# Kernel tuning notes

Hardware: AMD Instinct MI355X
Metric: run time of the kernel (lower is better)

Reference implementation:

```python
import jax, jax.numpy as jnp
import numpy as np

B, L, D = 2, 2048, 2048
NH, NKV = 16, 8
HD = D // NH            # 128
GQ = NH // NKV          # queries per kv head
THETA = 10000.0
SCALE = HD ** -0.5


def rope_tables(seq_len, dim, theta):
    inv_freq = 1.0 / theta ** (jnp.arange(0, dim, 2, dtype=jnp.float32) / dim)
    t = jnp.arange(seq_len, dtype=jnp.float32)
    freqs = jnp.outer(t, inv_freq)              # [L, dim/2]
    emb = jnp.concatenate([freqs, freqs], -1)   # [L, dim]
    return jnp.cos(emb), jnp.sin(emb)


def rotate_half(x):
    x1, x2 = jnp.split(x, 2, axis=-1)
    return jnp.concatenate([-x2, x1], -1)


def setup_inputs() -> dict:
    key = jax.random.key(0)
    ks = jax.random.split(key, 5)
    s = 0.02
    return {
        "x": jax.random.normal(ks[0], (B, L, D), jnp.float32),
        "Wq": jax.random.normal(ks[1], (NH * HD, D), jnp.float32) * s,
        "Wk": jax.random.normal(ks[2], (NKV * HD, D), jnp.float32) * s,
        "Wv": jax.random.normal(ks[3], (NKV * HD, D), jnp.float32) * s,
        "Wo": jax.random.normal(ks[4], (D, D), jnp.float32) * s,
    }


def reference(x, Wq, Wk, Wv, Wo):
    b, l, d = x.shape
    q = (x @ Wq.T).reshape(b, l, NH, HD).transpose(0, 2, 1, 3)    # [B,NH,L,HD]
    k = (x @ Wk.T).reshape(b, l, NKV, HD).transpose(0, 2, 1, 3)   # [B,NKV,L,HD]
    v = (x @ Wv.T).reshape(b, l, NKV, HD).transpose(0, 2, 1, 3)

    cos, sin = rope_tables(l, HD, THETA)                           # [L,HD]
    q = q * cos + rotate_half(q) * sin
    k = k * cos + rotate_half(k) * sin

    # GQA without materializing expanded K/V: group queries per kv head
    qg = q.reshape(b, NKV, GQ, l, HD)
    scores = jnp.einsum('bgrld,bgmd->bgrlm', qg, k) * SCALE        # [B,NKV,GQ,L,L]
    causal = jnp.triu(jnp.ones((l, l), bool), k=1)
    scores = jnp.where(causal, -jnp.inf, scores)
    attn = jax.nn.softmax(scores.astype(jnp.float32), axis=-1).astype(q.dtype)
    out = jnp.einsum('bgrlm,bgmd->bgrld', attn, v)                 # [B,NKV,GQ,L,HD]
    out = out.reshape(b, NH, l, HD).transpose(0, 2, 1, 3).reshape(b, l, d)
    return out @ Wo.T
```

## Files before the change

kernel.cpp:

```cpp
#include <hip/hip_runtime.h>
#include <cmath>

using u16 = unsigned short;
typedef u16    u16x4  __attribute__((ext_vector_type(4)));
typedef u16    u16x8  __attribute__((ext_vector_type(8)));
typedef __bf16 bf16x8 __attribute__((ext_vector_type(8)));
typedef float  f32x4  __attribute__((ext_vector_type(4)));

constexpr int Bc  = 2;
constexpr int Lc  = 2048;
constexpr int Dc  = 2048;
constexpr int NHc = 16;
constexpr int NKVc= 8;
constexpr int HDc = 128;

__device__ __forceinline__ u16 f2b(float f) {
  union { float f; unsigned u; } v; v.f = f;
  unsigned r = v.u + 0x7FFFu + ((v.u >> 16) & 1u);
  return (u16)(r >> 16);
}
__device__ __forceinline__ u16 f2b_fast(float f) {
  union { float f; unsigned u; } v; v.f = f;
  return (u16)((v.u + 0x8000u) >> 16);
}
__device__ __forceinline__ float b2f(u16 s) {
  union { unsigned u; float f; } v; v.u = ((unsigned)s) << 16;
  return v.f;
}
__device__ __forceinline__ bf16x8 ld_frag(const u16* p) {
  u16x8 u = *(const u16x8*)p;
  return __builtin_bit_cast(bf16x8, u);
}
__device__ __forceinline__ void gld_lds16(u16* ldst, const u16* gsrc) {
  __builtin_amdgcn_global_load_lds(
      (const __attribute__((address_space(1))) void*)gsrc,
      (__attribute__((address_space(3))) void*)ldst, 16, 0, 0);
}

__global__ void cvt_f32_bf16(const float* __restrict__ src, u16* __restrict__ dst, int n) {
  int i = (blockIdx.x * blockDim.x + threadIdx.x) * 4;
  if (i >= n) return;
  float4 v = *(const float4*)&src[i];
  u16x4 o = { f2b(v.x), f2b(v.y), f2b(v.z), f2b(v.w) };
  *(u16x4*)&dst[i] = o;
}

__global__ void cvt_w3(const float* __restrict__ Wq, const float* __restrict__ Wk,
                       const float* __restrict__ Wv, u16* __restrict__ dst) {
  const int n1 = Dc * Dc;
  const int n2 = n1 + (NKVc*HDc) * Dc;
  const int n3 = n2 + (NKVc*HDc) * Dc;
  int i = (blockIdx.x * blockDim.x + threadIdx.x) * 4;
  if (i >= n3) return;
  const float* src; int off;
  if (i < n1)      { src = Wq; off = i; }
  else if (i < n2) { src = Wk; off = i - n1; }
  else             { src = Wv; off = i - n2; }
  float4 v = *(const float4*)&src[off];
  u16x4 o = { f2b(v.x), f2b(v.y), f2b(v.z), f2b(v.w) };
  *(u16x4*)&dst[i] = o;
}

#define MFMA_(a, b, c) __builtin_amdgcn_mfma_f32_16x16x32_bf16(a, b, c, 0, 0, 0)
#define BAR()   __builtin_amdgcn_s_barrier()
#define SB0()   __builtin_amdgcn_sched_barrier(0)
#define LGKM0() { __asm__ volatile("s_waitcnt lgkmcnt(0)" ::: "memory"); \
                  __builtin_amdgcn_sched_barrier(0); }
#define VMC4()  __asm__ volatile("s_waitcnt vmcnt(4)" ::: "memory")
#define VMC2()  __asm__ volatile("s_waitcnt vmcnt(2)" ::: "memory")
#define VMC0()  __asm__ volatile("s_waitcnt vmcnt(0)" ::: "memory")
#define PRIO1() __builtin_amdgcn_s_setprio(1)
#define PRIO0() __builtin_amdgcn_s_setprio(0)

#define STG(lb, gp, goff, h, kc)                                          \
  { _Pragma("unroll")                                                     \
    for (int i_ = 0; i_ < 2; ++i_) {                                      \
      int c_ = wave + (i_ << 3);                                          \
      gld_lds16((lb) + (h) * 8192 + c_ * 512,                             \
                (gp) + (goff) + (size_t)(h) * 262144 + (size_t)c_ * 16384 + (kc)); } }

#define RD_ALO(rp) { _Pragma("unroll") for (int mi_ = 0; mi_ < 4; ++mi_) { \
    aLo[mi_][0] = ld_frag((rp) + mi_*1024 + cg0);                          \
    aLo[mi_][1] = ld_frag((rp) + mi_*1024 + cg1); } }
#define RD_AHI01(rp) { _Pragma("unroll") for (int mi_ = 0; mi_ < 2; ++mi_) { \
    aHi[mi_][0] = ld_frag((rp) + (4+mi_)*1024 + cg0);                        \
    aHi[mi_][1] = ld_frag((rp) + (4+mi_)*1024 + cg1); } }
#define RD_AHI23(rp) { _Pragma("unroll") for (int mi_ = 0; mi_ < 2; ++mi_) { \
    aHi[2+mi_][0] = ld_frag((rp) + (6+mi_)*1024 + cg0);                      \
    aHi[2+mi_][1] = ld_frag((rp) + (6+mi_)*1024 + cg1); } }
#define RD_BLO(rp) { _Pragma("unroll") for (int ni_ = 0; ni_ < 2; ++ni_) { \
    bLo[ni_][0] = ld_frag((rp) + ni_*1024 + cg0);                          \
    bLo[ni_][1] = ld_frag((rp) + ni_*1024 + cg1); } }
#define RD_BHI(rp) { _Pragma("unroll") for (int ni_ = 0; ni_ < 2; ++ni_) { \
    bHi[ni_][0] = ld_frag((rp) + (2+ni_)*1024 + cg0);                      \
    bHi[ni_][1] = ld_frag((rp) + (2+ni_)*1024 + cg1); } }

#define QMFMA(MI0, NI0, AX, BX)                                                \
  { _Pragma("unroll")                                                          \
    for (int mi_ = 0; mi_ < 4; ++mi_) {                                        \
      _Pragma("unroll")                                                        \
      for (int ni_ = 0; ni_ < 2; ++ni_) {                                      \
        acc[(MI0)+mi_][(NI0)+ni_] =                                            \
            MFMA_(AX[mi_][0], BX[ni_][0], acc[(MI0)+mi_][(NI0)+ni_]);          \
        acc[(MI0)+mi_][(NI0)+ni_] =                                            \
            MFMA_(AX[mi_][1], BX[ni_][1], acc[(MI0)+mi_][(NI0)+ni_]); } } }

__global__ __launch_bounds__(512, 2) void gemm256_qkv(
    const u16* __restrict__ A, const u16* __restrict__ W,
    u16* __restrict__ Qp, u16* __restrict__ Kp, u16* __restrict__ Vtp)
{
  __shared__ u16 lds[65536];
  const int tid  = threadIdx.x;
  const int wave = tid >> 6, lane = tid & 63;
  const int quad = lane >> 4, l16 = lane & 15, t7 = l16 & 7;
  const int bid = blockIdx.x;
  const int swz = (bid & 7) * 32 + (bid >> 3);
  const int tx = swz & 15, ty = swz >> 4;
  const int m0 = ty * 256, n0 = tx * 256;
  const int wm = wave >> 2, wn = wave & 3;
  const int srow = lane >> 3;
  const int sx8  = ((lane & 7) ^ srow) << 3;

  u16* const A0L = lds;
  u16* const B0L = lds + 16384;
  u16* const A1L = lds + 32768;
  u16* const B1L = lds + 49152;

  const size_t aOff = (size_t)(m0 + srow) * 2048 + sx8;
  const size_t bOff = (size_t)(n0 + srow) * 2048 + sx8;

  const int cg0 = ((quad ^ t7) << 3);
  const int cg1 = (((quad ^ t7) ^ 4) << 3);
  const u16* const rA0 = A0L + wm * 8192 + l16 * 64;
  const u16* const rA1 = A1L + wm * 8192 + l16 * 64;
  const u16* const rB0 = B0L + wn * 4096 + l16 * 64;
  const u16* const rB1 = B1L + wn * 4096 + l16 * 64;

  f32x4 acc[8][4];
#pragma unroll
  for (int i = 0; i < 8; ++i)
#pragma unroll
    for (int j = 0; j < 4; ++j) acc[i][j] = {0.f, 0.f, 0.f, 0.f};
  bf16x8 aLo[4][2], aHi[4][2], bLo[2][2], bHi[2][2];

  STG(A0L, A, aOff, 0, 0);  STG(A0L, A, aOff, 1, 0);
  STG(B0L, W, bOff, 0, 0);  STG(B0L, W, bOff, 1, 0);
  STG(A1L, A, aOff, 0, 64); STG(A1L, A, aOff, 1, 64);
  VMC4();
  BAR();
  RD_ALO(rA0); RD_BLO(rB0);
  LGKM0();

  for (int it = 0; it < 16; ++it) {
    const int t2 = it * 128;
    const bool g = (it < 15);
    RD_BHI(rB0); RD_AHI01(rA0);
    STG(B1L, W, bOff, 0, t2 + 64);
    SB0(); PRIO1(); QMFMA(0, 0, aLo, bLo); PRIO0(); LGKM0(); BAR();
    RD_AHI23(rA0);
    STG(B1L, W, bOff, 1, t2 + 64);
    VMC4();
    SB0(); PRIO1(); QMFMA(0, 2, aLo, bHi); PRIO0(); LGKM0(); BAR();
    RD_ALO(rA1);
    if (g) { STG(A0L, A, aOff, 0, t2 + 128); VMC2(); }
    else   { VMC0(); }
    SB0(); PRIO1(); QMFMA(4, 0, aHi, bLo); PRIO0(); LGKM0(); BAR();
    RD_BLO(rB1);
    if (g) STG(A0L, A, aOff, 1, t2 + 128);
    SB0(); PRIO1(); QMFMA(4, 2, aHi, bHi); PRIO0(); LGKM0(); BAR();
    RD_BHI(rB1); RD_AHI01(rA1);
    if (g) STG(B0L, W, bOff, 0, t2 + 128);
    SB0(); PRIO1(); QMFMA(0, 0, aLo, bLo); PRIO0(); LGKM0(); BAR();
    RD_AHI23(rA1);
    if (g) { STG(B0L, W, bOff, 1, t2 + 128); VMC4(); }
    SB0(); PRIO1(); QMFMA(0, 2, aLo, bHi); PRIO0(); LGKM0(); BAR();
    if (g) { RD_ALO(rA0); STG(A1L, A, aOff, 0, t2 + 192); VMC2(); }
    SB0(); PRIO1(); QMFMA(4, 0, aHi, bLo); PRIO0(); LGKM0(); BAR();
    if (g) { RD_BLO(rB0); STG(A1L, A, aOff, 1, t2 + 192); }
    SB0(); PRIO1(); QMFMA(4, 2, aHi, bHi); PRIO0(); LGKM0(); BAR();
  }

  if (n0 < 3072) {
    u16* Cb; int ldc, nc0;
    if (n0 < 2048) { Cb = Qp; ldc = 2048; nc0 = n0; }
    else           { Cb = Kp; ldc = 1024; nc0 = n0 - 2048; }
#pragma unroll
    for (int mi = 0; mi < 8; ++mi)
#pragma unroll
      for (int ni = 0; ni < 4; ++ni)
#pragma unroll
        for (int r = 0; r < 4; ++r) {
          int m = m0 + wm * 128 + mi * 16 + quad * 4 + r;
          int n = nc0 + wn * 64 + ni * 16 + l16;
          Cb[(size_t)m * ldc + n] = f2b(acc[mi][ni][r]);
        }
  } else {
    __syncthreads();
#pragma unroll
    for (int mi = 0; mi < 8; ++mi)
#pragma unroll
      for (int ni = 0; ni < 4; ++ni)
#pragma unroll
        for (int r = 0; r < 4; ++r) {
          int l = wm * 128 + mi * 16 + quad * 4 + r;
          int d = wn * 64 + ni * 16 + l16;
          int cgp = ((d >> 3) ^ (l & 31) ^ (l >> 5)) & 31;
          lds[l * 256 + (cgp << 3) + (d & 7)] = f2b(acc[mi][ni][r]);
        }
    __syncthreads();
    const int b    = m0 >> 11;
    const int hkv0 = (n0 - 3072) >> 7;
#pragma unroll
    for (int it2 = 0; it2 < 16; ++it2) {
      int sl = tid + it2 * 512;
      int dl = sl >> 5;
      int lc = (sl & 31) * 8;
      u16x8 v;
#pragma unroll
      for (int e = 0; e < 8; ++e) {
        int l = lc + e;
        int cgp = ((dl >> 3) ^ (l & 31) ^ (l >> 5)) & 31;
        v[e] = lds[l * 256 + (cgp << 3) + (dl & 7)];
      }
      const int hkv = hkv0 + (dl >> 7);
      const int d   = dl & 127;
      *(u16x8*)&Vtp[(((size_t)b * NKVc + hkv) * HDc + d) * (size_t)Lc + (m0 & (Lc - 1)) + lc] = v;
    }
  }
}
#undef STG
#undef RD_ALO
#undef RD_AHI01
#undef RD_AHI23
#undef RD_BLO
#undef RD_BHI
#undef QMFMA

__global__ __launch_bounds__(256) void gemm_out(
    const u16* __restrict__ A, const u16* __restrict__ W,
    float* __restrict__ Cf, int M, int N, int K)
{
  __shared__ u16 lds[16384];
  u16* lA = lds;
  u16* lB = lds + 8192;
  const int tid  = threadIdx.x;
  const int wave = tid >> 6, lane = tid & 63;
  const int quad = lane >> 4, l16 = lane & 15;
  const int t7   = l16 & 7;
  const int m0 = blockIdx.y * 128, n0 = blockIdx.x * 128;
  const int mw = (wave >> 1) * 64, nw = (wave & 1) * 64;
  const int r8 = lane >> 3;
  const int cgl = (lane & 7) ^ r8;

  f32x4 acc[4][4];
#pragma unroll
  for (int i = 0; i < 4; ++i)
#pragma unroll
    for (int j = 0; j < 4; ++j) acc[i][j] = {0.f, 0.f, 0.f, 0.f};

  for (int kt = 0; kt < K; kt += 64) {
#pragma unroll
    for (int cc = 0; cc < 4; ++cc) {
      int c = wave + cc * 4;
      gld_lds16(&lA[c * 512], &A[(size_t)(m0 + 8 * c + r8) * K + kt + cgl * 8]);
      gld_lds16(&lB[c * 512], &W[(size_t)(n0 + 8 * c + r8) * K + kt + cgl * 8]);
    }
    __syncthreads();
#pragma unroll
    for (int s = 0; s < 2; ++s) {
      bf16x8 af[4], bf[4];
#pragma unroll
      for (int i = 0; i < 4; ++i)
        af[i] = ld_frag(&lA[(mw + i*16 + l16) * 64 + ((quad + 4*s) ^ t7) * 8]);
#pragma unroll
      for (int j = 0; j < 4; ++j)
        bf[j] = ld_frag(&lB[(nw + j*16 + l16) * 64 + ((quad + 4*s) ^ t7) * 8]);
#pragma unroll
      for (int i = 0; i < 4; ++i)
#pragma unroll
        for (int j = 0; j < 4; ++j)
          acc[i][j] = __builtin_amdgcn_mfma_f32_16x16x32_bf16(af[i], bf[j], acc[i][j], 0, 0, 0);
    }
    __syncthreads();
  }

#pragma unroll
  for (int i = 0; i < 4; ++i)
#pragma unroll
    for (int j = 0; j < 4; ++j)
#pragma unroll
      for (int r = 0; r < 4; ++r) {
        int m = m0 + mw + i*16 + quad*4 + r;
        int n = n0 + nw + j*16 + l16;
        Cf[(size_t)m * N + n] = acc[i][j][r];
      }
}

__global__ void rope2_kernel(u16* __restrict__ Qp, u16* __restrict__ Kp, float qs)
{
  const int nQ = Bc * Lc * NHc * 64;
  const int nT = nQ + Bc * Lc * NKVc * 64;
  int t = blockIdx.x * blockDim.x + threadIdx.x;
  if (t >= nT) return;
  u16* T; int nheads; float osc; int idx;
  if (t < nQ) { T = Qp; nheads = NHc;  osc = qs;  idx = t; }
  else        { T = Kp; nheads = NKVc; osc = 1.f; idx = t - nQ; }
  int d   = idx & 63;
  int h   = (idx >> 6) % nheads;
  int row = idx / (nheads * 64);
  int l   = row & (Lc - 1);
  float freq = exp2f((float)d * (-13.287712379549449f / 64.f));
  float ang  = (float)l * freq;
  float s, c;
  sincosf(ang, &s, &c);
  size_t base = (size_t)row * (nheads * 128) + h * 128;
  float x1 = b2f(T[base + d]);
  float x2 = b2f(T[base + d + 64]);
  T[base + d]      = f2b((x1 * c - x2 * s) * osc);
  T[base + d + 64] = f2b((x2 * c + x1 * s) * osc);
}

__global__ __launch_bounds__(512) void flash_kernel(
    const u16* __restrict__ Q, const u16* __restrict__ K, const u16* __restrict__ Vt,
    u16* __restrict__ O)
{
  __shared__ u16 smem[41984];
  const int tid  = threadIdx.x;
  const int wave = tid >> 6, lane = tid & 63;
  const int quad = lane >> 4, l16 = lane & 15;
  const int hw = wave >> 2, wr = wave & 3;
  const int bhkv = blockIdx.x;
  const int b = bhkv >> 3, hkv = bhkv & 7;
  const int h = hkv * 2 + hw;

  const size_t kbase = ((size_t)b * Lc) * (NKVc * HDc) + (size_t)hkv * HDc;
  const size_t vbase = (((size_t)b * NKVc + hkv) * HDc) * (size_t)Lc;

  const int kr8 = lane >> 4;
  const int kcl = lane & 15;
  const int vr16 = lane >> 3;
  const int vkl  = lane & 7;

  u16* sP_w = smem + 32768 + wave * 1152;

  for (int pass = 0; pass < 2; ++pass) {
    const int qt = (pass == 0) ? (31 - (int)blockIdx.y) : (int)blockIdx.y;
    const int q0 = qt * 64;

    __syncthreads();
#pragma unroll
    for (int i = 0; i < 4; ++i) {
      int g = tid + i * 512;
      int row = g >> 4, cg = g & 15;
      int qh = hkv * 2 + (row >> 6);
      int rr = row & 63;
      *(u16x8*)&smem[row * 128 + (cg ^ (row & 15)) * 8] =
          *(const u16x8*)&Q[((size_t)(b * Lc + q0 + rr)) * Dc + (size_t)qh * HDc + cg * 8];
    }
    __syncthreads();
    bf16x8 qf[4];
#pragma unroll
    for (int ks = 0; ks < 4; ++ks)
      qf[ks] = ld_frag(&smem[(hw*64 + wr*16 + l16) * 128 + ((ks*4 + quad) ^ l16) * 8]);
    __syncthreads();

#pragma unroll
    for (int i = 0; i < 2; ++i) {
      int c = wave + i * 8;
      int row = c * 4 + kr8;
      gld_lds16(smem + c * 512,
                &K[kbase + (size_t)row * (NKVc*HDc) + (size_t)(kcl ^ (row & 15)) * 8]);
    }
#pragma unroll
    for (int i = 0; i < 2; ++i) {
      int c = wave + i * 8;
      int d = c * 8 + vr16;
      gld_lds16(smem + 16384 + c * 512,
                &Vt[vbase + (size_t)d * Lc + (size_t)(vkl ^ (d & 7)) * 8]);
    }

    f32x4 acc_o[8];
#pragma unroll
    for (int i = 0; i < 8; ++i) acc_o[i] = {0.f, 0.f, 0.f, 0.f};
    float ps[4] = {0.f, 0.f, 0.f, 0.f};

    for (int kt = 0; kt <= qt; ++kt) {
      const int kOff  = (kt & 1) ? 8192 : 0;
      const int kOffN = (kt & 1) ? 0 : 8192;
      const int vOff  = (kt & 1) ? 24576 : 16384;
      const int vOffN = (kt & 1) ? 16384 : 24576;

      __asm__ volatile("s_waitcnt vmcnt(2)\n\ts_barrier" ::: "memory");

      if (kt < qt) {
#pragma unroll
        for (int i = 0; i < 2; ++i) {
          int c = wave + i * 8;
          int row = (kt + 1) * 64 + c * 4 + kr8;
          gld_lds16(smem + kOffN + c * 512,
                    &K[kbase + (size_t)row * (NKVc*HDc) + (size_t)(kcl ^ (row & 15)) * 8]);
        }
      }

      const u16* sKc = smem + kOff;
      f32x4 accs[4];
#pragma unroll
      for (int n = 0; n < 4; ++n) accs[n] = {0.f, 0.f, 0.f, 0.f};
#pragma unroll
      for (int ks = 0; ks < 4; ++ks)
#pragma unroll
        for (int n = 0; n < 4; ++n) {
          bf16x8 kf = ld_frag(&sKc[(n*16 + l16) * 128 + ((ks*4 + quad) ^ l16) * 8]);
          accs[n] = __builtin_amdgcn_mfma_f32_16x16x32_bf16(qf[ks], kf, accs[n], 0, 0, 0);
        }

      const int qrow = q0 + wr*16 + quad*4;
      if (kt == qt) {
#pragma unroll
        for (int n = 0; n < 4; ++n) {
          int kg = kt*64 + n*16 + l16;
#pragma unroll
          for (int r = 0; r < 4; ++r)
            if (kg > qrow + r) accs[n][r] = -INFINITY;
        }
      }
#pragma unroll
      for (int n = 0; n < 4; ++n)
#pragma unroll
        for (int r = 0; r < 4; ++r) {
          float p = exp2f(accs[n][r]);
          accs[n][r] = p;
          ps[r] += p;
        }

#pragma unroll
      for (int n = 0; n < 4; ++n)
#pragma unroll
        for (int r = 0; r < 4; ++r)
          sP_w[(quad*4 + r) * 72 + n*16 + l16] = f2b_fast(accs[n][r]);

      if (kt < qt)
        __asm__ volatile("s_waitcnt vmcnt(2) lgkmcnt(0)\n\ts_barrier" ::: "memory");
      else
        __asm__ volatile("s_waitcnt vmcnt(0) lgkmcnt(0)\n\ts_barrier" ::: "memory");

      if (kt < qt) {
#pragma unroll
        for (int i = 0; i < 2; ++i) {
          int c = wave + i * 8;
          int d = c * 8 + vr16;
          gld_lds16(smem + vOffN + c * 512,
                    &Vt[vbase + (size_t)d * Lc + (kt+1)*64 + (size_t)(vkl ^ (d & 7)) * 8]);
        }
      }

      const u16* sVc = smem + vOff;
#pragma unroll
      for (int s2 = 0; s2 < 2; ++s2) {
        bf16x8 pf = ld_frag(&sP_w[l16 * 72 + s2*32 + quad*8]);
#pragma unroll
        for (int di = 0; di < 8; ++di) {
          bf16x8 vf = ld_frag(&sVc[(di*16 + l16) * 64 + ((s2*4 + quad) ^ (l16 & 7)) * 8]);
          acc_o[di] = __builtin_amdgcn_mfma_f32_16x16x32_bf16(pf, vf, acc_o[di], 0, 0, 0);
        }
      }
    }

#pragma unroll
    for (int off = 1; off < 16; off <<= 1)
#pragma unroll
      for (int r = 0; r < 4; ++r) ps[r] += __shfl_xor(ps[r], off);
    float inv[4];
#pragma unroll
    for (int r = 0; r < 4; ++r) inv[r] = 1.0f / ps[r];

#pragma unroll
    for (int di = 0; di < 8; ++di)
#pragma unroll
      for (int r = 0; r < 4; ++r) {
        int qrow = q0 + wr*16 + quad*4 + r;
        int d = di*16 + l16;
        float v = acc_o[di][r] * inv[r];
        O[((size_t)(b * Lc + qrow)) * Dc + (size_t)h * HDc + d] = f2b(v);
      }
  }
}

extern "C" void kernel_launch(void* const* d_in, const int* in_sizes, int n_in,
                              void* d_out, int out_size, void* d_ws, size_t ws_size,
                              hipStream_t stream)
{
  const float* x  = (const float*)d_in[0];
  const float* Wq = (const float*)d_in[1];
  const float* Wk = (const float*)d_in[2];
  const float* Wv = (const float*)d_in[3];
  const float* Wo = (const float*)d_in[4];
  float* out = (float*)d_out;

  const int M = Bc * Lc;
  u16* ws = (u16*)d_ws;
  u16* xb   = ws;
  u16* Ow   = xb;
  u16* Wcat = ws + (size_t)8 * 1024 * 1024;
  u16* Wob  = Wcat;
  u16* Qw   = Wcat + (size_t)8 * 1024 * 1024;
  u16* Kw   = Qw   + (size_t)8 * 1024 * 1024;
  u16* Vt   = Kw   + (size_t)4 * 1024 * 1024;

  const int nx = M * Dc;
  const int nq = Dc * Dc;
  const int nw3 = nq + 2 * (NKVc*HDc) * Dc;
  cvt_f32_bf16<<<nx/1024, 256, 0, stream>>>(x, xb, nx);
  cvt_w3<<<nw3/1024, 256, 0, stream>>>(Wq, Wk, Wv, Wcat);

  gemm256_qkv<<<256, 512, 0, stream>>>(xb, Wcat, Qw, Kw, Vt);

  const float qs = 0.08838834764831845f * 1.4426950408889634f;
  const int nrope = M * (NHc + NKVc) * 64;
  rope2_kernel<<<(nrope + 255) / 256, 256, 0, stream>>>(Qw, Kw, qs);

  flash_kernel<<<dim3(Bc*NKVc, 16), 512, 0, stream>>>(Qw, Kw, Vt, Ow);

  cvt_f32_bf16<<<nq/1024, 256, 0, stream>>>(Wo, Wob, nq);
  gemm_out<<<dim3(16, 32), 256, 0, stream>>>(Ow, Wob, out, M, Dc, Dc);
}
```

Baseline: 314.5 us.

## Restructure QKV GEMM main loop ping-pong schedule of LDS reads and global stages

Reorders the software pipeline in the 256-tile QKV GEMM. The prologue now preloads B for both k-halves before A, each k-half issues its LDS fragment reads at the start, and the barrier and waitcnt placement changes so each MFMA quarter waits for its own fragments (lgkmcnt(8), then 0 after the barrier). The aim is better overlap of LDS reads and global-to-LDS loads with MFMA work and fewer stalls at barriers. The risk is a race or hazard on LDS buffer reuse, or more exposed latency if the new wait points are stricter.

```diff
diff --git a/kernel.cpp b/kernel.cpp
--- a/kernel.cpp
+++ b/kernel.cpp
@@ -66,8 +66,8 @@
 #define SB0()   __builtin_amdgcn_sched_barrier(0)
 #define LGKM0() { __asm__ volatile("s_waitcnt lgkmcnt(0)" ::: "memory"); \
                   __builtin_amdgcn_sched_barrier(0); }
+#define LGKM8() __asm__ volatile("s_waitcnt lgkmcnt(8)" ::: "memory")
 #define VMC4()  __asm__ volatile("s_waitcnt vmcnt(4)" ::: "memory")
-#define VMC2()  __asm__ volatile("s_waitcnt vmcnt(2)" ::: "memory")
 #define VMC0()  __asm__ volatile("s_waitcnt vmcnt(0)" ::: "memory")
 #define PRIO1() __builtin_amdgcn_s_setprio(1)
 #define PRIO0() __builtin_amdgcn_s_setprio(0)
@@ -82,12 +82,9 @@
 #define RD_ALO(rp) { _Pragma("unroll") for (int mi_ = 0; mi_ < 4; ++mi_) { \
     aLo[mi_][0] = ld_frag((rp) + mi_*1024 + cg0);                          \
     aLo[mi_][1] = ld_frag((rp) + mi_*1024 + cg1); } }
-#define RD_AHI01(rp) { _Pragma("unroll") for (int mi_ = 0; mi_ < 2; ++mi_) { \
-    aHi[mi_][0] = ld_frag((rp) + (4+mi_)*1024 + cg0);                        \
+#define RD_AHI(rp) { _Pragma("unroll") for (int mi_ = 0; mi_ < 4; ++mi_) { \
+    aHi[mi_][0] = ld_frag((rp) + (4+mi_)*1024 + cg0);                      \
     aHi[mi_][1] = ld_frag((rp) + (4+mi_)*1024 + cg1); } }
-#define RD_AHI23(rp) { _Pragma("unroll") for (int mi_ = 0; mi_ < 2; ++mi_) { \
-    aHi[2+mi_][0] = ld_frag((rp) + (6+mi_)*1024 + cg0);                      \
-    aHi[2+mi_][1] = ld_frag((rp) + (6+mi_)*1024 + cg1); } }
 #define RD_BLO(rp) { _Pragma("unroll") for (int ni_ = 0; ni_ < 2; ++ni_) { \
     bLo[ni_][0] = ld_frag((rp) + ni_*1024 + cg0);                          \
     bLo[ni_][1] = ld_frag((rp) + ni_*1024 + cg1); } }
@@ -143,41 +140,49 @@
     for (int j = 0; j < 4; ++j) acc[i][j] = {0.f, 0.f, 0.f, 0.f};
   bf16x8 aLo[4][2], aHi[4][2], bLo[2][2], bHi[2][2];
 
+  STG(B0L, W, bOff, 0, 0);  STG(B0L, W, bOff, 1, 0);
   STG(A0L, A, aOff, 0, 0);  STG(A0L, A, aOff, 1, 0);
-  STG(B0L, W, bOff, 0, 0);  STG(B0L, W, bOff, 1, 0);
-  STG(A1L, A, aOff, 0, 64); STG(A1L, A, aOff, 1, 64);
+  STG(B1L, W, bOff, 0, 64); STG(B1L, W, bOff, 1, 64);
   VMC4();
   BAR();
-  RD_ALO(rA0); RD_BLO(rB0);
-  LGKM0();
 
   for (int it = 0; it < 16; ++it) {
-    const int t2 = it * 128;
+    const int kc = it * 128;
     const bool g = (it < 15);
-    RD_BHI(rB0); RD_AHI01(rA0);
-    STG(B1L, W, bOff, 0, t2 + 64);
-    SB0(); PRIO1(); QMFMA(0, 0, aLo, bLo); PRIO0(); LGKM0(); BAR();
-    RD_AHI23(rA0);
-    STG(B1L, W, bOff, 1, t2 + 64);
-    VMC4();
-    SB0(); PRIO1(); QMFMA(0, 2, aLo, bHi); PRIO0(); LGKM0(); BAR();
-    RD_ALO(rA1);
-    if (g) { STG(A0L, A, aOff, 0, t2 + 128); VMC2(); }
-    else   { VMC0(); }
-    SB0(); PRIO1(); QMFMA(4, 0, aHi, bLo); PRIO0(); LGKM0(); BAR();
-    RD_BLO(rB1);
-    if (g) STG(A0L, A, aOff, 1, t2 + 128);
-    SB0(); PRIO1(); QMFMA(4, 2, aHi, bHi); PRIO0(); LGKM0(); BAR();
-    RD_BHI(rB1); RD_AHI01(rA1);
-    if (g) STG(B0L, W, bOff, 0, t2 + 128);
-    SB0(); PRIO1(); QMFMA(0, 0, aLo, bLo); PRIO0(); LGKM0(); BAR();
-    RD_AHI23(rA1);
-    if (g) { STG(B0L, W, bOff, 1, t2 + 128); VMC4(); }
-    SB0(); PRIO1(); QMFMA(0, 2, aLo, bHi); PRIO0(); LGKM0(); BAR();
-    if (g) { RD_ALO(rA0); STG(A1L, A, aOff, 0, t2 + 192); VMC2(); }
-    SB0(); PRIO1(); QMFMA(4, 0, aHi, bLo); PRIO0(); LGKM0(); BAR();
-    if (g) { RD_BLO(rB0); STG(A1L, A, aOff, 1, t2 + 192); }
-    SB0(); PRIO1(); QMFMA(4, 2, aHi, bHi); PRIO0(); LGKM0(); BAR();
+    RD_ALO(rA0); RD_BLO(rB0);
+    STG(A1L, A, aOff, 0, kc + 64);
+    LGKM8(); SB0(); BAR(); LGKM0();
+    PRIO1(); QMFMA(0, 0, aLo, bLo); PRIO0(); BAR();
+    RD_BHI(rB0);
+    STG(A1L, A, aOff, 1, kc + 64);
+    SB0(); BAR(); LGKM0();
+    PRIO1(); QMFMA(0, 2, aLo, bHi); PRIO0(); BAR();
+    RD_AHI(rA0);
+    if (g) STG(B0L, W, bOff, 0, kc + 128);
+    SB0(); BAR(); LGKM0();
+    PRIO1(); QMFMA(4, 0, aHi, bLo); PRIO0(); BAR();
+    if (g) STG(B0L, W, bOff, 1, kc + 128);
+    SB0(); BAR();
+    PRIO1(); QMFMA(4, 2, aHi, bHi); PRIO0();
+    if (g) { VMC4(); } else { VMC0(); }
+    BAR();
+    RD_ALO(rA1); RD_BLO(rB1);
+    if (g) STG(A0L, A, aOff, 0, kc + 128);
+    LGKM8(); SB0(); BAR(); LGKM0();
+    PRIO1(); QMFMA(0, 0, aLo, bLo); PRIO0(); BAR();
+    RD_BHI(rB1);
+    if (g) STG(A0L, A, aOff, 1, kc + 128);
+    SB0(); BAR(); LGKM0();
+    PRIO1(); QMFMA(0, 2, aLo, bHi); PRIO0(); BAR();
+    RD_AHI(rA1);
+    if (g) STG(B1L, W, bOff, 0, kc + 192);
+    SB0(); BAR(); LGKM0();
+    PRIO1(); QMFMA(4, 0, aHi, bLo); PRIO0(); BAR();
+    if (g) STG(B1L, W, bOff, 1, kc + 192);
+    SB0(); BAR();
+    PRIO1(); QMFMA(4, 2, aHi, bHi); PRIO0();
+    if (g) VMC4();
+    BAR();
   }
 
   if (n0 < 3072) {
@@ -230,8 +235,7 @@
 }
 #undef STG
 #undef RD_ALO
-#undef RD_AHI01
-#undef RD_AHI23
+#undef RD_AHI
 #undef RD_BLO
 #undef RD_BHI
 #undef QMFMA
```

After: 298.6 us. 5.1% less time.
